# Kernel tuning notes

Measured on AMD Instinct MI355X. Metric: run time of the kernel, lower is better.

Reference implementation:

```python
import jax, jax.numpy as jnp
import numpy as np

PAD_IDX = 0        # assumed padding index (not defined in source snippet)
LAMBDA = 1.0       # lambda_bias buffer value
B, S, D, H = 2, 2048, 1024, 16
HD = D // H        # head_dim = 64
SCALE = HD ** -0.5


def setup_inputs() -> dict:
    key = jax.random.key(0)
    ks = jax.random.split(key, 18)
    w = lambda k: jax.random.normal(k, (D, D), jnp.float32) * 0.02
    b = lambda k: jax.random.normal(k, (D,), jnp.float32) * 0.02
    return {
        "query": jax.random.normal(ks[0], (B, S, D), jnp.float32),
        "key":   jax.random.normal(ks[1], (B, S, D), jnp.float32),
        "value": jax.random.normal(ks[2], (B, S, D), jnp.float32),
        # minval=1 for field_ids so no token is PAD -> no all--inf softmax rows
        "field_ids":      jax.random.randint(ks[3], (B, S), 1, 32),
        "entity_ids":     jax.random.randint(ks[4], (B, S), 0, 64),
        "time_ids":       jax.random.randint(ks[5], (B, S), 0, 128),
        "token_type_ids": jax.random.randint(ks[6], (B, S), 0, 8),
        "edge_ids":       jax.random.randint(ks[7], (B, S), 0, 4),
        "role_ids":       jax.random.randint(ks[8], (B, S), 0, 8),
        "Wq": w(ks[9]),  "bq": b(ks[10]),
        "Wk": w(ks[11]), "bk": b(ks[12]),
        "Wv": w(ks[13]), "bv": b(ks[14]),
        "Wo": w(ks[15]), "bo": b(ks[16]),
    }


def _bias_matrix(field_ids, entity_ids, time_ids, token_type_ids, edge_ids, role_ids):
    # pairwise equality bias, shape [B, S, S]
    eq = lambda x: (x[:, :, None] == x[:, None, :]).astype(jnp.float32)
    has_edge = ((edge_ids[:, :, None] != PAD_IDX) | (edge_ids[:, None, :] != PAD_IDX)).astype(jnp.float32)
    bias = (eq(field_ids)
            + eq(entity_ids)
            + 0.5 * eq(time_ids)
            + 0.3 * eq(token_type_ids)
            + 1.5 * has_edge
            + 0.5 * eq(role_ids))
    is_pad = field_ids == PAD_IDX
    pad_mask = is_pad[:, :, None] | is_pad[:, None, :]
    return jnp.where(pad_mask, -jnp.inf, bias)


def reference(query, key, value, field_ids, entity_ids, time_ids, token_type_ids,
              edge_ids, role_ids, Wq, bq, Wk, bk, Wv, bv, Wo, bo):
    Bsz, Sq, _ = query.shape
    Q = (query @ Wq.T + bq).reshape(Bsz, Sq, H, HD)
    K = (key   @ Wk.T + bk).reshape(Bsz, Sq, H, HD)
    V = (value @ Wv.T + bv).reshape(Bsz, Sq, H, HD)
    # [B, H, S, S]
    scores = jnp.einsum('bihd,bjhd->bhij', Q, K) * SCALE
    B_struct = _bias_matrix(field_ids, entity_ids, time_ids, token_type_ids, edge_ids, role_ids)
    scores = scores + LAMBDA * B_struct[:, None, :, :]
    attn = jax.nn.softmax(scores, axis=-1)
    out = jnp.einsum('bhij,bjhd->bihd', attn, V).reshape(Bsz, Sq, D)
    return out @ Wo.T + bo
```

## Files before the change

kernel.cpp:

```cpp
#include <hip/hip_runtime.h>
#include <hip/hip_bf16.h>
#include <stdint.h>

#define B_N 2
#define S_N 2048
#define D_N 1024
#define H_N 16
#define LOG2E 1.44269504f

using bf8    = __attribute__((ext_vector_type(8))) short;
using f32x4  = __attribute__((ext_vector_type(4))) float;
using f32x16 = __attribute__((ext_vector_type(16))) float;

static __device__ __forceinline__ ushort f2b(float f) {
  uint32_t u = __builtin_bit_cast(uint32_t, f);
  u += 0x7fffu + ((u >> 16) & 1u);
  return (ushort)(u >> 16);
}

static __device__ __forceinline__ uint32_t cvtpk(float a, float b) {
  uint32_t r;
  asm("v_cvt_pk_bf16_f32 %0, %1, %2" : "=v"(r) : "v"(a), "v"(b));
  return r;
}

typedef __attribute__((address_space(1))) const uint32_t GU32;
typedef __attribute__((address_space(3))) uint32_t LU32;
static __device__ __forceinline__ void gload16(const void* g, void* l) {
  __builtin_amdgcn_global_load_lds((GU32*)g, (LU32*)l, 16, 0, 0);
}

__global__ __launch_bounds__(256) void cvt3_kernel(const float* __restrict__ a, const float* __restrict__ b,
                                                   const float* __restrict__ c, ushort* __restrict__ oa,
                                                   ushort* __restrict__ ob, ushort* __restrict__ oc) {
  const float* s; ushort* d;
  if (blockIdx.y == 0) { s = a; d = oa; }
  else if (blockIdx.y == 1) { s = b; d = ob; }
  else { s = c; d = oc; }
  int i = (blockIdx.x * 256 + threadIdx.x) * 4;
  float4 v = *(const float4*)(s + i);
  ushort4 o;
  o.x = f2b(v.x); o.y = f2b(v.y); o.z = f2b(v.z); o.w = f2b(v.w);
  *(ushort4*)(d + i) = o;
}

__global__ __launch_bounds__(256) void cvt4_kernel(const float* __restrict__ a, const float* __restrict__ b,
                                                   const float* __restrict__ c, const float* __restrict__ e,
                                                   ushort* __restrict__ oa, ushort* __restrict__ ob,
                                                   ushort* __restrict__ oc, ushort* __restrict__ oe) {
  const float* s; ushort* d;
  if (blockIdx.y == 0) { s = a; d = oa; }
  else if (blockIdx.y == 1) { s = b; d = ob; }
  else if (blockIdx.y == 2) { s = c; d = oc; }
  else { s = e; d = oe; }
  int i = (blockIdx.x * 256 + threadIdx.x) * 4;
  float4 v = *(const float4*)(s + i);
  ushort4 o;
  o.x = f2b(v.x); o.y = f2b(v.y); o.z = f2b(v.z); o.w = f2b(v.w);
  *(ushort4*)(d + i) = o;
}

__global__ __launch_bounds__(256) void pack_codes_kernel(
    const int* __restrict__ f, const int* __restrict__ e, const int* __restrict__ ti,
    const int* __restrict__ tt, const int* __restrict__ ed, const int* __restrict__ ro,
    uint32_t* __restrict__ codes, int n) {
  int i = blockIdx.x * 256 + threadIdx.x;
  if (i >= n) return;
  uint32_t c = ((uint32_t)f[i] & 31u) | (((uint32_t)e[i] & 63u) << 5) |
               (((uint32_t)ti[i] & 127u) << 11) | (((uint32_t)tt[i] & 7u) << 18) |
               (((uint32_t)ro[i] & 7u) << 21) |
               ((ed[i] != 0) ? (1u << 24) : 0u) | ((f[i] == 0) ? (1u << 25) : 0u);
  codes[i] = c;
}

static __device__ __forceinline__ float bias_val(uint32_t a, uint32_t b) {
  uint32_t x = a ^ b;
  uint32_t o = a | b;
  float v = (o & 0x1000000u) ? 1.5f : 0.0f;
  v += (x & 0x1Fu)     ? 0.0f : 1.0f;
  v += (x & 0x7E0u)    ? 0.0f : 1.0f;
  v += (x & 0x3F800u)  ? 0.0f : 0.5f;
  v += (x & 0x1C0000u) ? 0.0f : 0.3f;
  v += (x & 0xE00000u) ? 0.0f : 0.5f;
  return (o & 0x2000000u) ? -30000.f : v;
}

__global__ __launch_bounds__(256) void bias_build(const uint32_t* __restrict__ codes,
                                                  float* __restrict__ BF) {
  int t = blockIdx.x * 256 + threadIdx.x;
  int lane = t & 63;
  int c    = (t >> 6) & 7;
  int kvt  = (t >> 9) & 31;
  int qtile = (t >> 14) & 63;
  int b    = (t >> 20) & 1;
  int q  = qtile * 32 + (lane & 31);
  int kv = kvt * 64 + (c >> 2) * 32 + (c & 3) * 8 + (lane >> 5) * 4;
  uint32_t cq = codes[b * S_N + q];
  uint4 cj = *(const uint4*)(codes + b * S_N + kv);
  float4 o;
  o.x = bias_val(cq, cj.x) * LOG2E - 16.0f;
  o.y = bias_val(cq, cj.y) * LOG2E - 16.0f;
  o.z = bias_val(cq, cj.z) * LOG2E - 16.0f;
  o.w = bias_val(cq, cj.w) * LOG2E - 16.0f;
  *(float4*)(BF + (size_t)t * 4) = o;
}

template <int MODE>
static __device__ __forceinline__ void gemm_core(ushort* As, ushort* Bs,
    const ushort* __restrict__ A, const ushort* __restrict__ W, const float* __restrict__ bias,
    void* __restrict__ out, float scale) {
  const int tid = threadIdx.x, lane = tid & 63, wid = tid >> 6;
  const int g = lane >> 4, c = lane & 15;
  const int wm = wid >> 1, wn = wid & 1;
  const int m0 = blockIdx.y * 128, n0 = blockIdx.x * 128;

  f32x4 acc[4][4];
#pragma unroll
  for (int i = 0; i < 4; ++i)
#pragma unroll
    for (int j = 0; j < 4; ++j) acc[i][j] = (f32x4){0.f, 0.f, 0.f, 0.f};

  for (int k0 = 0; k0 < D_N; k0 += 32) {
#pragma unroll
    for (int j = 0; j < 2; ++j) {
      int idx = tid + j * 256;
      int row = idx >> 2, c8 = (idx & 3) * 8;
      gload16(A + (size_t)(m0 + row) * D_N + k0 + c8, As + idx * 8);
      gload16(W + (size_t)(n0 + row) * D_N + k0 + c8, Bs + idx * 8);
    }
    __syncthreads();
    bf8 af[4], bw[4];
#pragma unroll
    for (int mi = 0; mi < 4; ++mi) af[mi] = *(const bf8*)(As + (wm * 64 + mi * 16 + c) * 32 + g * 8);
#pragma unroll
    for (int ni = 0; ni < 4; ++ni) bw[ni] = *(const bf8*)(Bs + (wn * 64 + ni * 16 + c) * 32 + g * 8);
#pragma unroll
    for (int mi = 0; mi < 4; ++mi)
#pragma unroll
      for (int ni = 0; ni < 4; ++ni)
        acc[mi][ni] = __builtin_amdgcn_mfma_f32_16x16x32_bf16(af[mi], bw[ni], acc[mi][ni], 0, 0, 0);
    __syncthreads();
  }

#pragma unroll
  for (int mi = 0; mi < 4; ++mi)
#pragma unroll
    for (int ni = 0; ni < 4; ++ni) {
      int ncol = n0 + wn * 64 + ni * 16 + c;
      float bv = bias[ncol];
      int hh = ncol >> 6, dd = ncol & 63;
      if (MODE == 2) {
        int mb = m0 + wm * 64 + mi * 16 + g * 4;
        int bb = mb >> 11, kv = mb & 2047;
        int kvt = kv >> 6, kin = kv & 63;
        int ks = kin >> 4, hif = (kin >> 3) & 1, e = kin & 7;
        int jj = dd >> 5, l31v = dd & 31;
        int lanef = hif * 32 + l31v;
        size_t off = (((size_t)(bb * H_N + hh) * 32 + kvt) * 8 + ks * 2 + jj) * 512 + lanef * 8 + e;
        ushort4 o4;
        o4.x = f2b((acc[mi][ni][0] + bv) * scale);
        o4.y = f2b((acc[mi][ni][1] + bv) * scale);
        o4.z = f2b((acc[mi][ni][2] + bv) * scale);
        o4.w = f2b((acc[mi][ni][3] + bv) * scale);
        *(ushort4*)((ushort*)out + off) = o4;
      } else {
#pragma unroll
        for (int r = 0; r < 4; ++r) {
          int m = m0 + wm * 64 + mi * 16 + g * 4 + r;
          float v = (acc[mi][ni][r] + bv) * scale;
          if (MODE == 0) {
            int bb = m >> 11, q = m & 2047;
            int qtile = q >> 5, l31q = q & 31;
            int ks = dd >> 4, hif = (dd >> 3) & 1, e = dd & 7;
            int lanef = hif * 32 + l31q;
            size_t off = (((size_t)(bb * H_N + hh) * 64 + qtile) * 4 + ks) * 512 + lanef * 8 + e;
            ((ushort*)out)[off] = f2b(v);
          } else if (MODE == 3) {
            int bb = m >> 11, s = m & 2047;
            int kvt = s >> 6, sin = s & 63;
            int jj = sin >> 5, l31k = sin & 31;
            int ks = dd >> 4, hif = (dd >> 3) & 1, e = dd & 7;
            int lanef = hif * 32 + l31k;
            size_t off = (((size_t)(bb * H_N + hh) * 32 + kvt) * 8 + ks * 2 + jj) * 512 + lanef * 8 + e;
            ((ushort*)out)[off] = f2b(v);
          } else {
            ((float*)out)[(size_t)m * D_N + ncol] = v;
          }
        }
      }
    }
}

__global__ __launch_bounds__(256) void gemm_qkv(
    const ushort* __restrict__ Xq, const ushort* __restrict__ Xk, const ushort* __restrict__ Xv,
    const ushort* __restrict__ Wq, const ushort* __restrict__ Wk, const ushort* __restrict__ Wv,
    const float* __restrict__ bq, const float* __restrict__ bk, const float* __restrict__ bv,
    ushort* __restrict__ Qo, ushort* __restrict__ Ko, ushort* __restrict__ Vo) {
  __shared__ __align__(16) ushort As[128 * 32];
  __shared__ __align__(16) ushort Bs[128 * 32];
  if (blockIdx.z == 0)      gemm_core<0>(As, Bs, Xq, Wq, bq, Qo, 0.125f * LOG2E);
  else if (blockIdx.z == 1) gemm_core<3>(As, Bs, Xk, Wk, bk, Ko, 1.0f);
  else                      gemm_core<2>(As, Bs, Xv, Wv, bv, Vo, 1.0f);
}

__global__ __launch_bounds__(256) void gemm_o(const ushort* __restrict__ A, const ushort* __restrict__ W,
                                              const float* __restrict__ bias, float* __restrict__ out) {
  __shared__ __align__(16) ushort As[128 * 32];
  __shared__ __align__(16) ushort Bs[128 * 32];
  gemm_core<1>(As, Bs, A, W, bias, out, 1.0f);
}

__global__ __launch_bounds__(256, 2) void attn_kernel(const ushort* __restrict__ QF, const ushort* __restrict__ KF,
                                                      const ushort* __restrict__ VF, const float* __restrict__ BF,
                                                      ushort* __restrict__ AO) {
  const int tid = threadIdx.x, lane = tid & 63, w = tid >> 6;
  const int l31 = lane & 31, hi = lane >> 5;
  const int raw = blockIdx.x;
  const int bh = (raw & 7) * 4 + ((raw >> 3) & 3);
  const int x  = raw >> 5;
  const int b = bh >> 4, h = bh & 15;
  const int qtile = x * 4 + w;

  const ushort* Qp = QF + ((size_t)(bh * 64 + qtile) * 4) * 512 + lane * 8;
  bf8 aq[4];
#pragma unroll
  for (int ks = 0; ks < 4; ++ks) aq[ks] = *(const bf8*)(Qp + ks * 512);

  const ushort* Ku = KF + (size_t)bh * 32 * 8 * 512;
  const ushort* Vu = VF + (size_t)bh * 32 * 8 * 512;
  const float*  Bu = BF + (size_t)(b * 64 + qtile) * 32 * 2048;
  const int koff = lane * 8;
  const int boff = lane * 4;

  float lr = 0.f;
  f32x16 o0, o1;
#pragma unroll
  for (int r = 0; r < 16; ++r) { o0[r] = 0.f; o1[r] = 0.f; }

  const int CROW0[16] = {0,1,2,3, 8,9,10,11, 16,17,18,19, 24,25,26,27};

  auto LOADK = [&](bf8 (&kf)[4][2], int t) {
    const ushort* p = Ku + (size_t)t * 4096 + koff;
#pragma unroll
    for (int ks = 0; ks < 4; ++ks) {
      kf[ks][0] = *(const bf8*)(p + (ks * 2 + 0) * 512);
      kf[ks][1] = *(const bf8*)(p + (ks * 2 + 1) * 512);
    }
  };
  auto LOADV = [&](bf8 (&vf)[4][2], int t) {
    const ushort* p = Vu + (size_t)t * 4096 + koff;
#pragma unroll
    for (int ks = 0; ks < 4; ++ks) {
      vf[ks][0] = *(const bf8*)(p + (ks * 2 + 0) * 512);
      vf[ks][1] = *(const bf8*)(p + (ks * 2 + 1) * 512);
    }
  };
  auto LOADB = [&](float4 (&bb)[8], int t) {
    const float* p = Bu + (size_t)t * 2048 + boff;
#pragma unroll
    for (int c = 0; c < 8; ++c)
      bb[c] = *(const float4*)(p + c * 256);
  };

  auto TILE = [&](const bf8 (&kf)[4][2], const bf8 (&vf)[4][2], const float4 (&bb)[8]) {
    f32x16 s0, s1;
#pragma unroll
    for (int g = 0; g < 4; ++g) {
      s0[g * 4 + 0] = bb[g].x;     s0[g * 4 + 1] = bb[g].y;
      s0[g * 4 + 2] = bb[g].z;     s0[g * 4 + 3] = bb[g].w;
      s1[g * 4 + 0] = bb[4 + g].x; s1[g * 4 + 1] = bb[4 + g].y;
      s1[g * 4 + 2] = bb[4 + g].z; s1[g * 4 + 3] = bb[4 + g].w;
    }
    __builtin_amdgcn_s_setprio(1);
#pragma unroll
    for (int ks = 0; ks < 4; ++ks) {
      s0 = __builtin_amdgcn_mfma_f32_32x32x16_bf16(kf[ks][0], aq[ks], s0, 0, 0, 0);
      s1 = __builtin_amdgcn_mfma_f32_32x32x16_bf16(kf[ks][1], aq[ks], s1, 0, 0, 0);
    }
    __builtin_amdgcn_s_setprio(0);

#pragma unroll
    for (int r = 0; r < 16; ++r) {
      s0[r] = __builtin_exp2f(s0[r]);
      s1[r] = __builtin_exp2f(s1[r]);
    }
    float a8[8];
#pragma unroll
    for (int r = 0; r < 8; ++r)
      a8[r] = (s0[r] + s0[r + 8]) + (s1[r] + s1[r + 8]);
    lr += ((a8[0] + a8[4]) + (a8[1] + a8[5])) + ((a8[2] + a8[6]) + (a8[3] + a8[7]));

    bf8 pa[4];
#pragma unroll
    for (int t = 0; t < 2; ++t) {
      uint32_t wv[4][2];
#pragma unroll
      for (int g = 0; g < 4; ++g) {
        const float* sp = (t == 0) ? (const float*)&s0 : (const float*)&s1;
        wv[g][0] = cvtpk(sp[g * 4 + 0], sp[g * 4 + 1]);
        wv[g][1] = cvtpk(sp[g * 4 + 2], sp[g * 4 + 3]);
      }
#pragma unroll
      for (int pr = 0; pr < 2; ++pr) {
        uint32_t x0 = hi ? wv[2 * pr][0] : wv[2 * pr + 1][0];
        uint32_t x1 = hi ? wv[2 * pr][1] : wv[2 * pr + 1][1];
        uint32_t r0 = (uint32_t)__shfl_xor((int)x0, 32);
        uint32_t r1 = (uint32_t)__shfl_xor((int)x1, 32);
        uint4 pw;
        pw.x = hi ? r0 : wv[2 * pr][0];
        pw.y = hi ? r1 : wv[2 * pr][1];
        pw.z = hi ? wv[2 * pr + 1][0] : r0;
        pw.w = hi ? wv[2 * pr + 1][1] : r1;
        pa[t * 2 + pr] = __builtin_bit_cast(bf8, pw);
      }
    }

    __builtin_amdgcn_s_setprio(1);
#pragma unroll
    for (int ks = 0; ks < 4; ++ks) {
      o0 = __builtin_amdgcn_mfma_f32_32x32x16_bf16(pa[ks], vf[ks][0], o0, 0, 0, 0);
      o1 = __builtin_amdgcn_mfma_f32_32x32x16_bf16(pa[ks], vf[ks][1], o1, 0, 0, 0);
    }
    __builtin_amdgcn_s_setprio(0);
  };

  bf8 kA[4][2], kB[4][2], vC[4][2];
  float4 bA[8], bB[8];
  LOADK(kA, 0); LOADB(bA, 0);

#pragma unroll 1
  for (int p = 0; p < 15; ++p) {
    int t = 2 * p;
    LOADK(kB, t + 1); LOADB(bB, t + 1); LOADV(vC, t);
    TILE(kA, vC, bA);
    LOADK(kA, t + 2); LOADB(bA, t + 2); LOADV(vC, t + 1);
    TILE(kB, vC, bB);
  }
  LOADK(kB, 31); LOADB(bB, 31); LOADV(vC, 30);
  TILE(kA, vC, bA);
  LOADV(vC, 31);
  TILE(kB, vC, bB);

  lr += __shfl_xor(lr, 32);
  float inv = 1.0f / lr;
#pragma unroll
  for (int r = 0; r < 16; ++r) {
    float ivr = __shfl(inv, CROW0[r] + 4 * hi);
    int q = qtile * 32 + CROW0[r] + 4 * hi;
    size_t base = ((size_t)b * S_N + q) * D_N + h * 64 + l31;
    AO[base]      = f2b(o0[r] * ivr);
    AO[base + 32] = f2b(o1[r] * ivr);
  }
}

extern "C" void kernel_launch(void* const* d_in, const int* in_sizes, int n_in,
                              void* d_out, int out_size, void* d_ws, size_t ws_size,
                              hipStream_t stream) {
  (void)in_sizes; (void)n_in; (void)out_size; (void)ws_size;
  const float* query = (const float*)d_in[0];
  const float* key_  = (const float*)d_in[1];
  const float* value = (const float*)d_in[2];
  const int* fid  = (const int*)d_in[3];
  const int* eid  = (const int*)d_in[4];
  const int* tmid = (const int*)d_in[5];
  const int* ttid = (const int*)d_in[6];
  const int* edid = (const int*)d_in[7];
  const int* rlid = (const int*)d_in[8];
  const float* Wq = (const float*)d_in[9];  const float* bq = (const float*)d_in[10];
  const float* Wk = (const float*)d_in[11]; const float* bk = (const float*)d_in[12];
  const float* Wv = (const float*)d_in[13]; const float* bv = (const float*)d_in[14];
  const float* Wo = (const float*)d_in[15]; const float* bo = (const float*)d_in[16];

  char* ws = (char*)d_ws;
  const size_t MB = 1024 * 1024;
  ushort* Xq  = (ushort*)(ws);
  ushort* Xk  = (ushort*)(ws + 8 * MB);
  ushort* Xv  = (ushort*)(ws + 16 * MB);
  ushort* Wqb = (ushort*)(ws + 24 * MB);
  ushort* Wkb = (ushort*)(ws + 26 * MB);
  ushort* Wvb = (ushort*)(ws + 28 * MB);
  float*  BF  = (float*)(ws);
  ushort* QFw = (ushort*)(ws + 34 * MB);
  ushort* KFw = (ushort*)(ws + 42 * MB);
  ushort* VFw = (ushort*)(ws + 50 * MB);
  ushort* AOw = (ushort*)(ws + 58 * MB);
  ushort* Wob = (ushort*)(ws + 66 * MB);
  uint32_t* codes = (uint32_t*)(ws + 68 * MB);

  const int MK = B_N * S_N * D_N;
  const int WK = D_N * D_N;
  cvt3_kernel<<<dim3(MK / 1024, 3), 256, 0, stream>>>(query, key_, value, Xq, Xk, Xv);
  cvt4_kernel<<<dim3(WK / 1024, 4), 256, 0, stream>>>(Wq, Wk, Wv, Wo, Wqb, Wkb, Wvb, Wob);
  pack_codes_kernel<<<(B_N * S_N) / 256, 256, 0, stream>>>(fid, eid, tmid, ttid, edid, rlid, codes, B_N * S_N);

  gemm_qkv<<<dim3(D_N / 128, (B_N * S_N) / 128, 3), 256, 0, stream>>>(
      Xq, Xk, Xv, Wqb, Wkb, Wvb, bq, bk, bv, QFw, KFw, VFw);
  bias_build<<<(B_N * S_N * S_N / 4) / 256, 256, 0, stream>>>(codes, BF);
  attn_kernel<<<512, 256, 0, stream>>>(QFw, KFw, VFw, BF, AOw);
  gemm_o<<<dim3(D_N / 128, (B_N * S_N) / 128), 256, 0, stream>>>(AOw, Wob, bo, (float*)d_out);
}
```

Measured before the change: 164.2 us.

## Store bias matrix as fp16 and fuse conversion prep kernels into one launch

The precomputed attention bias matrix is now stored in fp16 instead of fp32, which halves its write traffic in bias_build and its read traffic in the attention kernel. The attention loop now loads four 16-byte fp16 vectors per tile and converts them to float in registers. The -16 offset previously folded into the bias is dropped. The three input-conversion and code-packing kernels are merged into one prep_kernel launch to cut launch overhead. Bias values lose precision in fp16, and removing the offset changes the exp2 range, so overflow is a risk if scores get large.

```diff
diff --git a/kernel.cpp b/kernel.cpp
--- a/kernel.cpp
+++ b/kernel.cpp
@@ -9,6 +9,7 @@
 #define LOG2E 1.44269504f
 
 using bf8    = __attribute__((ext_vector_type(8))) short;
+using us8    = __attribute__((ext_vector_type(8))) unsigned short;
 using f32x4  = __attribute__((ext_vector_type(4))) float;
 using f32x16 = __attribute__((ext_vector_type(16))) float;
 
@@ -24,53 +25,56 @@
   return r;
 }
 
+static __device__ __forceinline__ float h2f(ushort u) {
+  return (float)__builtin_bit_cast(_Float16, u);
+}
+
+static __device__ __forceinline__ ushort h16(float x) {
+  return __builtin_bit_cast(ushort, (_Float16)x);
+}
+
 typedef __attribute__((address_space(1))) const uint32_t GU32;
 typedef __attribute__((address_space(3))) uint32_t LU32;
 static __device__ __forceinline__ void gload16(const void* g, void* l) {
   __builtin_amdgcn_global_load_lds((GU32*)g, (LU32*)l, 16, 0, 0);
 }
 
-__global__ __launch_bounds__(256) void cvt3_kernel(const float* __restrict__ a, const float* __restrict__ b,
-                                                   const float* __restrict__ c, ushort* __restrict__ oa,
-                                                   ushort* __restrict__ ob, ushort* __restrict__ oc) {
-  const float* s; ushort* d;
-  if (blockIdx.y == 0) { s = a; d = oa; }
-  else if (blockIdx.y == 1) { s = b; d = ob; }
-  else { s = c; d = oc; }
-  int i = (blockIdx.x * 256 + threadIdx.x) * 4;
+static __device__ __forceinline__ void cvt4B(const float* __restrict__ s, ushort* __restrict__ d, int i) {
   float4 v = *(const float4*)(s + i);
   ushort4 o;
   o.x = f2b(v.x); o.y = f2b(v.y); o.z = f2b(v.z); o.w = f2b(v.w);
   *(ushort4*)(d + i) = o;
 }
 
-__global__ __launch_bounds__(256) void cvt4_kernel(const float* __restrict__ a, const float* __restrict__ b,
-                                                   const float* __restrict__ c, const float* __restrict__ e,
-                                                   ushort* __restrict__ oa, ushort* __restrict__ ob,
-                                                   ushort* __restrict__ oc, ushort* __restrict__ oe) {
-  const float* s; ushort* d;
-  if (blockIdx.y == 0) { s = a; d = oa; }
-  else if (blockIdx.y == 1) { s = b; d = ob; }
-  else if (blockIdx.y == 2) { s = c; d = oc; }
-  else { s = e; d = oe; }
-  int i = (blockIdx.x * 256 + threadIdx.x) * 4;
-  float4 v = *(const float4*)(s + i);
-  ushort4 o;
-  o.x = f2b(v.x); o.y = f2b(v.y); o.z = f2b(v.z); o.w = f2b(v.w);
-  *(ushort4*)(d + i) = o;
-}
-
-__global__ __launch_bounds__(256) void pack_codes_kernel(
+__global__ __launch_bounds__(256) void prep_kernel(
+    const float* __restrict__ q, const float* __restrict__ k, const float* __restrict__ v,
+    const float* __restrict__ wq, const float* __restrict__ wk, const float* __restrict__ wv,
+    const float* __restrict__ wo,
+    ushort* __restrict__ oq, ushort* __restrict__ ok, ushort* __restrict__ ov,
+    ushort* __restrict__ owq, ushort* __restrict__ owk, ushort* __restrict__ owv,
+    ushort* __restrict__ owo,
     const int* __restrict__ f, const int* __restrict__ e, const int* __restrict__ ti,
     const int* __restrict__ tt, const int* __restrict__ ed, const int* __restrict__ ro,
-    uint32_t* __restrict__ codes, int n) {
-  int i = blockIdx.x * 256 + threadIdx.x;
-  if (i >= n) return;
-  uint32_t c = ((uint32_t)f[i] & 31u) | (((uint32_t)e[i] & 63u) << 5) |
-               (((uint32_t)ti[i] & 127u) << 11) | (((uint32_t)tt[i] & 7u) << 18) |
-               (((uint32_t)ro[i] & 7u) << 21) |
-               ((ed[i] != 0) ? (1u << 24) : 0u) | ((f[i] == 0) ? (1u << 25) : 0u);
-  codes[i] = c;
+    uint32_t* __restrict__ codes) {
+  int x = blockIdx.x;
+  if (x < 12288) {
+    int which = x >> 12, i = (x & 4095) * 1024 + threadIdx.x * 4;
+    const float* s = (which == 0) ? q : (which == 1) ? k : v;
+    ushort* d = (which == 0) ? oq : (which == 1) ? ok : ov;
+    cvt4B(s, d, i);
+  } else if (x < 16384) {
+    int which = (x - 12288) >> 10, i = (x & 1023) * 1024 + threadIdx.x * 4;
+    const float* s = (which == 0) ? wq : (which == 1) ? wk : (which == 2) ? wv : wo;
+    ushort* d = (which == 0) ? owq : (which == 1) ? owk : (which == 2) ? owv : owo;
+    cvt4B(s, d, i);
+  } else {
+    int i = (x - 16384) * 256 + threadIdx.x;
+    uint32_t c = ((uint32_t)f[i] & 31u) | (((uint32_t)e[i] & 63u) << 5) |
+                 (((uint32_t)ti[i] & 127u) << 11) | (((uint32_t)tt[i] & 7u) << 18) |
+                 (((uint32_t)ro[i] & 7u) << 21) |
+                 ((ed[i] != 0) ? (1u << 24) : 0u) | ((f[i] == 0) ? (1u << 25) : 0u);
+    codes[i] = c;
+  }
 }
 
 static __device__ __forceinline__ float bias_val(uint32_t a, uint32_t b) {
@@ -86,23 +90,30 @@
 }
 
 __global__ __launch_bounds__(256) void bias_build(const uint32_t* __restrict__ codes,
-                                                  float* __restrict__ BF) {
+                                                  ushort* __restrict__ BF) {
   int t = blockIdx.x * 256 + threadIdx.x;
-  int lane = t & 63;
-  int c    = (t >> 6) & 7;
-  int kvt  = (t >> 9) & 31;
-  int qtile = (t >> 14) & 63;
-  int b    = (t >> 20) & 1;
+  int v8    = t & 1;
+  int lane  = (t >> 1) & 63;
+  int h     = (t >> 7) & 1;
+  int kvt   = (t >> 8) & 31;
+  int qtile = (t >> 13) & 63;
+  int b     = t >> 19;
+  int hi = lane >> 5;
   int q  = qtile * 32 + (lane & 31);
-  int kv = kvt * 64 + (c >> 2) * 32 + (c & 3) * 8 + (lane >> 5) * 4;
   uint32_t cq = codes[b * S_N + q];
-  uint4 cj = *(const uint4*)(codes + b * S_N + kv);
-  float4 o;
-  o.x = bias_val(cq, cj.x) * LOG2E - 16.0f;
-  o.y = bias_val(cq, cj.y) * LOG2E - 16.0f;
-  o.z = bias_val(cq, cj.z) * LOG2E - 16.0f;
-  o.w = bias_val(cq, cj.w) * LOG2E - 16.0f;
-  *(float4*)(BF + (size_t)t * 4) = o;
+  int kvb = kvt * 64 + h * 32 + v8 * 16 + hi * 4;
+  uint4 c0 = *(const uint4*)(codes + b * S_N + kvb);
+  uint4 c1 = *(const uint4*)(codes + b * S_N + kvb + 8);
+  ushort o[8];
+  o[0] = h16(bias_val(cq, c0.x) * LOG2E);
+  o[1] = h16(bias_val(cq, c0.y) * LOG2E);
+  o[2] = h16(bias_val(cq, c0.z) * LOG2E);
+  o[3] = h16(bias_val(cq, c0.w) * LOG2E);
+  o[4] = h16(bias_val(cq, c1.x) * LOG2E);
+  o[5] = h16(bias_val(cq, c1.y) * LOG2E);
+  o[6] = h16(bias_val(cq, c1.z) * LOG2E);
+  o[7] = h16(bias_val(cq, c1.w) * LOG2E);
+  *(uint4*)(BF + (size_t)t * 8) = *(const uint4*)o;
 }
 
 template <int MODE>
@@ -211,7 +222,7 @@
 }
 
 __global__ __launch_bounds__(256, 2) void attn_kernel(const ushort* __restrict__ QF, const ushort* __restrict__ KF,
-                                                      const ushort* __restrict__ VF, const float* __restrict__ BF,
+                                                      const ushort* __restrict__ VF, const ushort* __restrict__ BF,
                                                       ushort* __restrict__ AO) {
   const int tid = threadIdx.x, lane = tid & 63, w = tid >> 6;
   const int l31 = lane & 31, hi = lane >> 5;
@@ -228,9 +239,9 @@
 
   const ushort* Ku = KF + (size_t)bh * 32 * 8 * 512;
   const ushort* Vu = VF + (size_t)bh * 32 * 8 * 512;
-  const float*  Bu = BF + (size_t)(b * 64 + qtile) * 32 * 2048;
+  const ushort* Bu = BF + (size_t)(b * 64 + qtile) * 32 * 2048;
   const int koff = lane * 8;
-  const int boff = lane * 4;
+  const int boff = lane * 16;
 
   float lr = 0.f;
   f32x16 o0, o1;
@@ -255,22 +266,23 @@
       vf[ks][1] = *(const bf8*)(p + (ks * 2 + 1) * 512);
     }
   };
-  auto LOADB = [&](float4 (&bb)[8], int t) {
-    const float* p = Bu + (size_t)t * 2048 + boff;
-#pragma unroll
-    for (int c = 0; c < 8; ++c)
-      bb[c] = *(const float4*)(p + c * 256);
+  auto LOADB = [&](us8 (&bb)[4], int t) {
+    const ushort* p = Bu + (size_t)t * 2048 + boff;
+    bb[0] = *(const us8*)(p);
+    bb[1] = *(const us8*)(p + 8);
+    bb[2] = *(const us8*)(p + 1024);
+    bb[3] = *(const us8*)(p + 1024 + 8);
   };
 
-  auto TILE = [&](const bf8 (&kf)[4][2], const bf8 (&vf)[4][2], const float4 (&bb)[8]) {
+  auto TILE = [&](const bf8 (&kf)[4][2], const bf8 (&vf)[4][2], const us8 (&bb)[4]) {
     f32x16 s0, s1;
 #pragma unroll
-    for (int g = 0; g < 4; ++g) {
-      s0[g * 4 + 0] = bb[g].x;     s0[g * 4 + 1] = bb[g].y;
-      s0[g * 4 + 2] = bb[g].z;     s0[g * 4 + 3] = bb[g].w;
-      s1[g * 4 + 0] = bb[4 + g].x; s1[g * 4 + 1] = bb[4 + g].y;
-      s1[g * 4 + 2] = bb[4 + g].z; s1[g * 4 + 3] = bb[4 + g].w;
-    }
+    for (int g = 0; g < 4; ++g)
+#pragma unroll
+      for (int j = 0; j < 4; ++j) {
+        s0[g * 4 + j] = h2f(bb[g >> 1][(g & 1) * 4 + j]);
+        s1[g * 4 + j] = h2f(bb[2 + (g >> 1)][(g & 1) * 4 + j]);
+      }
     __builtin_amdgcn_s_setprio(1);
 #pragma unroll
     for (int ks = 0; ks < 4; ++ks) {
@@ -325,7 +337,7 @@
   };
 
   bf8 kA[4][2], kB[4][2], vC[4][2];
-  float4 bA[8], bB[8];
+  us8 bA[4], bB[4];
   LOADK(kA, 0); LOADB(bA, 0);
 
 #pragma unroll 1
@@ -379,23 +391,20 @@
   ushort* Wqb = (ushort*)(ws + 24 * MB);
   ushort* Wkb = (ushort*)(ws + 26 * MB);
   ushort* Wvb = (ushort*)(ws + 28 * MB);
-  float*  BF  = (float*)(ws);
-  ushort* QFw = (ushort*)(ws + 34 * MB);
-  ushort* KFw = (ushort*)(ws + 42 * MB);
-  ushort* VFw = (ushort*)(ws + 50 * MB);
-  ushort* AOw = (ushort*)(ws + 58 * MB);
-  ushort* Wob = (ushort*)(ws + 66 * MB);
-  uint32_t* codes = (uint32_t*)(ws + 68 * MB);
-
-  const int MK = B_N * S_N * D_N;
-  const int WK = D_N * D_N;
-  cvt3_kernel<<<dim3(MK / 1024, 3), 256, 0, stream>>>(query, key_, value, Xq, Xk, Xv);
-  cvt4_kernel<<<dim3(WK / 1024, 4), 256, 0, stream>>>(Wq, Wk, Wv, Wo, Wqb, Wkb, Wvb, Wob);
-  pack_codes_kernel<<<(B_N * S_N) / 256, 256, 0, stream>>>(fid, eid, tmid, ttid, edid, rlid, codes, B_N * S_N);
-
+  ushort* BF  = (ushort*)(ws);
+  ushort* QFw = (ushort*)(ws + 30 * MB);
+  ushort* KFw = (ushort*)(ws + 38 * MB);
+  ushort* VFw = (ushort*)(ws + 46 * MB);
+  ushort* AOw = (ushort*)(ws + 54 * MB);
+  ushort* Wob = (ushort*)(ws + 62 * MB);
+  uint32_t* codes = (uint32_t*)(ws + 64 * MB);
+
+  prep_kernel<<<16400, 256, 0, stream>>>(query, key_, value, Wq, Wk, Wv, Wo,
+                                         Xq, Xk, Xv, Wqb, Wkb, Wvb, Wob,
+                                         fid, eid, tmid, ttid, edid, rlid, codes);
   gemm_qkv<<<dim3(D_N / 128, (B_N * S_N) / 128, 3), 256, 0, stream>>>(
       Xq, Xk, Xv, Wqb, Wkb, Wvb, bq, bk, bv, QFw, KFw, VFw);
-  bias_build<<<(B_N * S_N * S_N / 4) / 256, 256, 0, stream>>>(codes, BF);
+  bias_build<<<4096, 256, 0, stream>>>(codes, BF);
   attn_kernel<<<512, 256, 0, stream>>>(QFw, KFw, VFw, BF, AOw);
   gemm_o<<<dim3(D_N / 128, (B_N * S_N) / 128), 256, 0, stream>>>(AOw, Wob, bo, (float*)d_out);
 }
```

Result: faster. 156.5 us (-4.7%).
